# Kernel tuning notes

Hardware: AMD Instinct MI355X
Metric: run time of the kernel (lower is better)

## Reference

```python
import jax, jax.numpy as jnp
import numpy as np

DIM = 1024
HEADS = 16
DIM_HEAD = 64
INNER = HEADS * DIM_HEAD  # 1024
B, N = 4, 1024
SCALE = DIM_HEAD ** -0.5


def _layernorm(t, g, b, eps=1e-5):
    mu = jnp.mean(t, axis=-1, keepdims=True)
    var = jnp.var(t, axis=-1, keepdims=True)
    return (t - mu) * jax.lax.rsqrt(var + eps) * g + b


def setup_inputs() -> dict:
    key = jax.random.key(0)
    ks = jax.random.split(key, 8)
    return {
        "x": jax.random.normal(ks[0], (B, N, DIM), dtype=jnp.float32),
        "y": jax.random.normal(ks[1], (B, N, DIM), dtype=jnp.float32),
        "gx": jnp.ones((DIM,), jnp.float32),
        "bx": jnp.zeros((DIM,), jnp.float32),
        "gy": jnp.ones((DIM,), jnp.float32),
        "by": jnp.zeros((DIM,), jnp.float32),
        "Wqkv_x": jax.random.normal(ks[2], (DIM, 3 * INNER), jnp.float32) * 0.02,
        "Wqkv_y": jax.random.normal(ks[3], (DIM, 3 * INNER), jnp.float32) * 0.02,
        "Wout_x": jax.random.normal(ks[4], (INNER, DIM), jnp.float32) * 0.02,
        "bout_x": jnp.zeros((DIM,), jnp.float32),
        "Wout_y": jax.random.normal(ks[5], (INNER, DIM), jnp.float32) * 0.02,
        "bout_y": jnp.zeros((DIM,), jnp.float32),
    }


def _split_heads(t):
    b, n, _ = t.shape
    return t.reshape(b, n, HEADS, DIM_HEAD).transpose(0, 2, 1, 3)  # b h n d


def reference(x, y, gx, bx, gy, by, Wqkv_x, Wqkv_y, Wout_x, bout_x, Wout_y, bout_y):
    xn = _layernorm(x, gx, bx)
    yn = _layernorm(y, gy, by)
    qx, kx, vx = [_split_heads(t) for t in jnp.split(xn @ Wqkv_x, 3, axis=-1)]
    qy, ky, vy = [_split_heads(t) for t in jnp.split(yn @ Wqkv_y, 3, axis=-1)]
    # concat along HEADS dim -> 2h heads; each stream's heads attend within that stream
    q = jnp.concatenate([qx, qy], axis=1)
    k = jnp.concatenate([kx, ky], axis=1)
    v = jnp.concatenate([vx, vy], axis=1)
    dots = jnp.einsum('bhid,bhjd->bhij', q, k) * SCALE  # [B, 2h, N, N]
    attn = jax.nn.softmax(dots, axis=-1)
    out = jnp.einsum('bhij,bhjd->bhid', attn, v)  # [B, 2h, N, d]
    xo = out[:, :HEADS]  # original code uses the x-chunk for BOTH outputs (faithful)
    xo = xo.transpose(0, 2, 1, 3).reshape(xo.shape[0], xo.shape[2], INNER)  # b n (h d)
    out_x = xo @ Wout_x + bout_x
    out_y = xo @ Wout_y + bout_y
    return (out_x, out_y)
```

## Files before the change

kernel.cpp:

```cpp
#include <hip/hip_runtime.h>

typedef __attribute__((ext_vector_type(8))) short s16x8;
typedef __attribute__((ext_vector_type(4))) float f32x4;
typedef unsigned short u16;

#define DEV __device__ __forceinline__

DEV u16 f2bf(float f) {
    unsigned u = __builtin_bit_cast(unsigned, f);
    unsigned r = u + 0x7fffu + ((u >> 16) & 1u);
    return (u16)(r >> 16);
}

DEV float exp2a(float x) {
    float r;
    asm("v_exp_f32 %0, %1" : "=v"(r) : "v"(x));
    return r;
}

DEV unsigned cvtpk(float lo, float hi) {
    unsigned r;
    asm("v_cvt_pk_bf16_f32 %0, %1, %2" : "=v"(r) : "v"(lo), "v"(hi));
    return r;
}

DEV void gload_lds16(const void* g, void* l) {
    __builtin_amdgcn_global_load_lds(
        (const __attribute__((address_space(1))) unsigned int*)g,
        (__attribute__((address_space(3))) unsigned int*)l, 16, 0, 0);
}

DEV f32x4 mfma16(s16x8 a, s16x8 b, f32x4 c) {
    return __builtin_amdgcn_mfma_f32_16x16x32_bf16(a, b, c, 0, 0, 0);
}

template <int N>
DEV void vmwait() {
    asm volatile("s_waitcnt vmcnt(%0)" ::"n"(N) : "memory");
}

__global__ __launch_bounds__(256) void prep_kernel(
    const float* __restrict__ x, const float* __restrict__ g,
    const float* __restrict__ b, u16* __restrict__ xn,
    const float* __restrict__ Wqkv, const float* __restrict__ Woutx,
    const float* __restrict__ Wouty, u16* __restrict__ wqkv_t,
    u16* __restrict__ wout_t) {
    __shared__ float tile[64][68];
    const int t = threadIdx.x;
    const int bid = blockIdx.x;

    if (bid < 4096) {
        const int row = bid;
        const float4 v = *(const float4*)(x + (size_t)row * 1024 + t * 4);
        float s1 = v.x + v.y + v.z + v.w;
        float s2 = v.x * v.x + v.y * v.y + v.z * v.z + v.w * v.w;
#pragma unroll
        for (int d = 1; d < 64; d <<= 1) {
            s1 += __shfl_xor(s1, d);
            s2 += __shfl_xor(s2, d);
        }
        float* red = &tile[0][0];
        if ((t & 63) == 0) { red[(t >> 6) * 2] = s1; red[(t >> 6) * 2 + 1] = s2; }
        __syncthreads();
        s1 = red[0] + red[2] + red[4] + red[6];
        s2 = red[1] + red[3] + red[5] + red[7];
        const float mu = s1 * (1.0f / 1024.0f);
        const float var = s2 * (1.0f / 1024.0f) - mu * mu;
        const float rs = rsqrtf(var + 1e-5f);
        const float4 gv = *(const float4*)(g + t * 4);
        const float4 bv = *(const float4*)(b + t * 4);
        ushort4 o;
        o.x = f2bf((v.x - mu) * rs * gv.x + bv.x);
        o.y = f2bf((v.y - mu) * rs * gv.y + bv.y);
        o.z = f2bf((v.z - mu) * rs * gv.z + bv.z);
        o.w = f2bf((v.w - mu) * rs * gv.w + bv.w);
        *(ushort4*)(xn + (size_t)row * 1024 + t * 4) = o;
        return;
    }

    const float* src;
    u16* d0;
    int ld, n0, k0;
    if (bid < 4096 + 768) {
        const int idx = bid - 4096;
        src = Wqkv; d0 = wqkv_t; ld = 3072;
        n0 = (idx % 48) * 64; k0 = (idx / 48) * 64;
    } else {
        const int idx = bid - 4096 - 768;
        const int z = idx >> 8, rem = idx & 255;
        src = (z == 0) ? Woutx : Wouty;
        d0 = wout_t + (size_t)z * 1024 * 1024; ld = 1024;
        n0 = (rem & 15) * 64; k0 = (rem >> 4) * 64;
    }
    const int kl = t >> 4, nl = (t & 15) * 4;
#pragma unroll
    for (int p = 0; p < 4; ++p) {
        float4 v = *(const float4*)(src + (size_t)(k0 + kl + p * 16) * ld + n0 + nl);
        tile[kl + p * 16][nl + 0] = v.x;
        tile[kl + p * 16][nl + 1] = v.y;
        tile[kl + p * 16][nl + 2] = v.z;
        tile[kl + p * 16][nl + 3] = v.w;
    }
    __syncthreads();
    const int nl2 = t >> 2, kc = (t & 3) * 16;
    __align__(16) u16 tmp[16];
#pragma unroll
    for (int j = 0; j < 16; ++j) tmp[j] = f2bf(tile[kc + j][nl2]);
    u16* d = d0 + (size_t)(n0 + nl2) * 1024 + k0 + kc;
    ((uint4*)d)[0] = ((const uint4*)tmp)[0];
    ((uint4*)d)[1] = ((const uint4*)tmp)[1];
}

__global__ __launch_bounds__(512, 2) void gemm1k(const u16* __restrict__ A,
                                                 const u16* __restrict__ B,
                                                 u16* __restrict__ Qb, u16* __restrict__ Kb,
                                                 u16* __restrict__ Vt) {
    constexpr int MQ = 2, NQ = 3, HA = 32, HB = 48, TM = 64, TN = 96;
    constexpr int CHA = 1024, CHBF = 1536;
    constexpr int NI = 8;

    __shared__ __align__(16) u16 As[2 * 2 * CHA * 8];
    __shared__ __align__(16) u16 Bs[2 * CHBF * 8];

    const int tid = threadIdx.x, lane = tid & 63;
    const int wave = tid >> 6;
    const int wm = wave >> 1, wn = wave & 1;
    const int lr = lane & 15, cg = lane >> 4;

    const int bid = blockIdx.x;
    const int bid2 = (bid & 7) * 32 + (bid >> 3);
    const int bxi = bid2 & 15, byi = bid2 >> 4;
    const int m0 = byi * 256, n0 = bxi * 192;

    const u16* __restrict__ Ag = A + (size_t)m0 * 1024;
    const u16* __restrict__ Bg = B + (size_t)n0 * 1024;

    f32x4 acc[2 * MQ][2 * NQ] = {};

#define STG_A(b, h, t)                                                              \
    do {                                                                            \
        _Pragma("unroll") for (int u = 0; u < 2; ++u) {                             \
            const int idx = u * 512 + tid;                                          \
            const int loc = idx >> 3, pp = idx & 7;                                 \
            const int row = (loc & 127) | ((h)*128);                                \
            gload_lds16(Ag + (size_t)row * 1024 + (t)*64 + ((pp ^ (row & 7)) << 3), \
                        &As[(((b)*2 + (h)) * CHA + idx) * 8]);                      \
        }                                                                           \
    } while (0)
#define STG_B(b, t)                                                                 \
    do {                                                                            \
        _Pragma("unroll") for (int u = 0; u < 3; ++u) {                             \
            const int idx = u * 512 + tid;                                          \
            const int row = idx >> 3, pp = idx & 7;                                 \
            gload_lds16(Bg + (size_t)row * 1024 + (t)*64 + ((pp ^ (row & 7)) << 3), \
                        &Bs[((b)*CHBF + idx) * 8]);                                 \
        }                                                                           \
    } while (0)

#define LDA(bb, lm, dst)                                                            \
    _Pragma("unroll") for (int mf = 0; mf < MQ; ++mf)                               \
        _Pragma("unroll") for (int ks = 0; ks < 2; ++ks) {                          \
            const int grow = wm * 64 + (lm)*32 + mf * 16 + lr;                      \
            dst[mf][ks] = *(const s16x8*)&As[((((bb)*2 + (grow >> 7)) * CHA) +      \
                                              (grow & 127) * 8 +                    \
                                              ((cg + ks * 4) ^ (lr & 7))) * 8];     \
        }

#define LDB(bb, ln, dst)                                                            \
    _Pragma("unroll") for (int nf = 0; nf < NQ; ++nf)                               \
        _Pragma("unroll") for (int ks = 0; ks < 2; ++ks) {                          \
            const int rr = wn * TN + (ln)*HB + nf * 16 + lr;                        \
            dst[nf][ks] = *(const s16x8*)&Bs[((bb)*CHBF + rr * 8 +                  \
                                              ((cg + ks * 4) ^ (lr & 7))) * 8];     \
        }

#define MM(lm, ln, A_, B_)                                                          \
    __builtin_amdgcn_s_setprio(1);                                                  \
    _Pragma("unroll") for (int mf = 0; mf < MQ; ++mf)                               \
        _Pragma("unroll") for (int nf = 0; nf < NQ; ++nf)                           \
            _Pragma("unroll") for (int ks = 0; ks < 2; ++ks)                        \
                acc[(lm)*MQ + mf][(ln)*NQ + nf] = mfma16(                           \
                    A_[mf][ks], B_[nf][ks], acc[(lm)*MQ + mf][(ln)*NQ + nf]);       \
    __builtin_amdgcn_s_setprio(0);

#define BAR() asm volatile("s_barrier" ::: "memory")

    STG_A(0, 0, 0);
    STG_A(0, 1, 0);
    STG_B(0, 0);
    STG_A(1, 0, 1);
    STG_B(1, 1);
    vmwait<5>();
    BAR();

    s16x8 va[MQ][2];
    s16x8 vb0[NQ][2], vb1[NQ][2];

#pragma unroll 1
    for (int i = 0; i < NI - 1; ++i) {
        const int t1 = 2 * i + 1, t2 = 2 * i + 2, t3 = 2 * i + 3;
        LDA(0, 0, va); LDB(0, 0, vb0); STG_A(1, 1, t1); BAR(); MM(0, 0, va, vb0);
        LDB(0, 1, vb1);                                 BAR(); MM(0, 1, va, vb1);
        LDA(0, 1, va);                 STG_A(0, 0, t2); BAR(); MM(1, 0, va, vb0);
        STG_B(0, t2); vmwait<5>();                      BAR(); MM(1, 1, va, vb1);
        LDA(1, 0, va); LDB(1, 0, vb0); STG_A(0, 1, t2); BAR(); MM(0, 0, va, vb0);
        LDB(1, 1, vb1);                                 BAR(); MM(0, 1, va, vb1);
        LDA(1, 1, va);                 STG_A(1, 0, t3); BAR(); MM(1, 0, va, vb0);
        STG_B(1, t3); vmwait<5>();                      BAR(); MM(1, 1, va, vb1);
    }
    LDA(0, 0, va); LDB(0, 0, vb0); STG_A(1, 1, 15); BAR(); MM(0, 0, va, vb0);
    LDB(0, 1, vb1);                                 BAR(); MM(0, 1, va, vb1);
    LDA(0, 1, va);                                  BAR(); MM(1, 0, va, vb0);
    vmwait<0>();                                    BAR(); MM(1, 1, va, vb1);
    LDA(1, 0, va); LDB(1, 0, vb0); MM(0, 0, va, vb0);
    LDB(1, 1, vb1);                MM(0, 1, va, vb1);
    LDA(1, 1, va);                 MM(1, 0, va, vb0);
    MM(1, 1, va, vb1);

#undef STG_A
#undef STG_B
#undef LDA
#undef LDB
#undef MM
#undef BAR

#pragma unroll
    for (int am = 0; am < 2 * MQ; ++am) {
        const int lm = am / MQ, mf = am % MQ;
        const int rowb = m0 + wm * TM + lm * HA + mf * 16 + cg * 4;
        const int bb2 = rowb >> 10, ii = rowb & 1023;
#pragma unroll
        for (int an = 0; an < 2 * NQ; ++an) {
            const int ln = an / NQ, nf = an % NQ;
            const int col = n0 + wn * TN + ln * HB + nf * 16 + lr;
            const int which = col >> 10, hd = col & 1023;
            const int h = hd >> 6, dd = hd & 63;
            if (which == 2) {
                ushort4 pk;
                pk.x = f2bf(acc[am][an][0]);
                pk.y = f2bf(acc[am][an][1]);
                pk.z = f2bf(acc[am][an][2]);
                pk.w = f2bf(acc[am][an][3]);
                *(ushort4*)(Vt + (size_t)((bb2 << 4) + h) * 65536 + dd * 1024 + ii) = pk;
            } else {
                u16* dst = (which == 0) ? Qb : Kb;
                const float sc = (which == 0) ? 0.18033688011112042f : 1.0f;
#pragma unroll
                for (int r = 0; r < 4; ++r)
                    dst[(size_t)(((bb2 << 4) + h) * 1024 + ii + r) * 64 + dd] =
                        f2bf(acc[am][an][r] * sc);
            }
        }
    }
}

template <int BN, int WM, int EPI>
__global__ __launch_bounds__(512, 2) void gemm8(const u16* __restrict__ A,
                                                const u16* __restrict__ B,
                                                u16* __restrict__ Qb, u16* __restrict__ Kb,
                                                u16* __restrict__ Vb,
                                                const float* __restrict__ bx,
                                                const float* __restrict__ by,
                                                float* __restrict__ out, int NBX) {
    constexpr int BM = 256, WN = 8 / WM;
    constexpr int TM = BM / WM, TN = BN / WN;
    constexpr int MQ = TM / 32, NQ = TN / 32;
    constexpr int HA = TM / 2, HB = TN / 2;
    constexpr int CHA = 1024;
    constexpr int CHB = BN * 4;
    constexpr int GA = 2, GB = CHB / 512;
    constexpr int NI = 8;

    __shared__ __align__(16) u16 As[2 * 2 * CHA * 8];
    __shared__ __align__(16) u16 Bs[2 * 2 * CHB * 8];

    const int tid = threadIdx.x, lane = tid & 63;
    const int wave = tid >> 6;
    const int wm = wave / WN, wn = wave % WN;
    const int lr = lane & 15, cg = lane >> 4;

    const int nwg = NBX * 16;
    const int bid = blockIdx.x;
    const int bid2 = (bid & 7) * (nwg >> 3) + (bid >> 3);
    const int bxi = bid2 % NBX, byi = bid2 / NBX;
    const int m0 = byi * 256, n0 = bxi * BN;

    const u16* __restrict__ Ag = A + (size_t)m0 * 1024;
    const u16* __restrict__ Bg = B + (size_t)n0 * 1024;

    f32x4 acc[2 * MQ][2 * NQ] = {};

#define STG_A(b, h, t)                                                              \
    do {                                                                            \
        _Pragma("unroll") for (int u = 0; u < GA; ++u) {                            \
            const int idx = u * 512 + tid;                                          \
            const int loc = idx >> 3, pp = idx & 7;                                 \
            const int row = (loc & (HA - 1)) | ((h)*HA) | ((loc / HA) * 2 * HA);    \
            gload_lds16(Ag + (size_t)row * 1024 + (t)*64 + ((pp ^ (row & 7)) << 3), \
                        &As[(((b)*2 + (h)) * CHA + idx) * 8]);                      \
        }                                                                           \
    } while (0)
#define STG_B(b, h, t)                                                              \
    do {                                                                            \
        _Pragma("unroll") for (int u = 0; u < GB; ++u) {                            \
            const int idx = u * 512 + tid;                                          \
            const int loc = idx >> 3, pp = idx & 7;                                 \
            const int row = (loc & (HB - 1)) | ((h)*HB) | ((loc / HB) * 2 * HB);    \
            gload_lds16(Bg + (size_t)row * 1024 + (t)*64 + ((pp ^ (row & 7)) << 3), \
                        &Bs[(((b)*2 + (h)) * CHB + idx) * 8]);                      \
        }                                                                           \
    } while (0)

#define LDA(bb, lm, dst)                                                            \
    _Pragma("unroll") for (int mf = 0; mf < MQ; ++mf)                               \
        _Pragma("unroll") for (int ks = 0; ks < 2; ++ks)                            \
            dst[mf][ks] = *(const s16x8*)&As[((((bb)*2 + (lm)) * CHA) +             \
                                              (mf * 16 + lr + wm * HA) * 8 +        \
                                              ((cg + ks * 4) ^ (lr & 7))) * 8];

#define LDB(bb, ln, dst)                                                            \
    _Pragma("unroll") for (int nf = 0; nf < NQ; ++nf)                               \
        _Pragma("unroll") for (int ks = 0; ks < 2; ++ks)                            \
            dst[nf][ks] = *(const s16x8*)&Bs[((((bb)*2 + (ln)) * CHB) +             \
                                              (nf * 16 + lr + wn * HB) * 8 +        \
                                              ((cg + ks * 4) ^ (lr & 7))) * 8];

#define MM(lm, ln, A_, B_)                                                          \
    __builtin_amdgcn_s_setprio(1);                                                  \
    _Pragma("unroll") for (int mf = 0; mf < MQ; ++mf)                               \
        _Pragma("unroll") for (int nf = 0; nf < NQ; ++nf)                           \
            _Pragma("unroll") for (int ks = 0; ks < 2; ++ks)                        \
                acc[(lm)*MQ + mf][(ln)*NQ + nf] = mfma16(                           \
                    A_[mf][ks], B_[nf][ks], acc[(lm)*MQ + mf][(ln)*NQ + nf]);       \
    __builtin_amdgcn_s_setprio(0);

#define BAR() asm volatile("s_barrier" ::: "memory")

    STG_A(0, 0, 0);
    STG_A(0, 1, 0);
    STG_B(0, 0, 0);
    STG_B(0, 1, 0);
    STG_A(1, 0, 1);
    STG_B(1, 0, 1);
    vmwait<GA + GB>();
    BAR();

    s16x8 va[MQ][2];
    s16x8 vb0[NQ][2], vb1[NQ][2];

#pragma unroll 1
    for (int i = 0; i < NI - 1; ++i) {
        const int t1 = 2 * i + 1, t2 = 2 * i + 2, t3 = 2 * i + 3;
        LDA(0, 0, va); LDB(0, 0, vb0); STG_A(1, 1, t1); BAR(); MM(0, 0, va, vb0);
        LDB(0, 1, vb1);                STG_B(1, 1, t1); BAR(); MM(0, 1, va, vb1);
        LDA(0, 1, va);                 STG_A(0, 0, t2); BAR(); MM(1, 0, va, vb0);
        STG_B(0, 0, t2); vmwait<GA + GB>();             BAR(); MM(1, 1, va, vb1);
        LDA(1, 0, va); LDB(1, 0, vb0); STG_A(0, 1, t2); BAR(); MM(0, 0, va, vb0);
        LDB(1, 1, vb1);                STG_B(0, 1, t2); BAR(); MM(0, 1, va, vb1);
        LDA(1, 1, va);                 STG_A(1, 0, t3); BAR(); MM(1, 0, va, vb0);
        STG_B(1, 0, t3); vmwait<GA + GB>();             BAR(); MM(1, 1, va, vb1);
    }
    LDA(0, 0, va); LDB(0, 0, vb0); STG_A(1, 1, 15); BAR(); MM(0, 0, va, vb0);
    LDB(0, 1, vb1);                STG_B(1, 1, 15); BAR(); MM(0, 1, va, vb1);
    LDA(0, 1, va);                                  BAR(); MM(1, 0, va, vb0);
    vmwait<0>();                                    BAR(); MM(1, 1, va, vb1);
    LDA(1, 0, va); LDB(1, 0, vb0); MM(0, 0, va, vb0);
    LDB(1, 1, vb1);                MM(0, 1, va, vb1);
    LDA(1, 1, va);                 MM(1, 0, va, vb0);
    MM(1, 1, va, vb1);

#undef STG_A
#undef STG_B
#undef LDA
#undef LDB
#undef MM
#undef BAR

#pragma unroll
    for (int am = 0; am < 2 * MQ; ++am) {
        const int lm = am / MQ, mf = am % MQ;
        const int rowb = m0 + wm * TM + lm * HA + mf * 16 + cg * 4;
#pragma unroll
        for (int an = 0; an < 2 * NQ; ++an) {
            const int ln = an / NQ, nf = an % NQ;
            const int col = n0 + wn * TN + ln * HB + nf * 16 + lr;
            if (EPI == 0) {
                const int which = col >> 10, hd = col & 1023;
                const int h = hd >> 6, dd = hd & 63;
                u16* dst = (which == 0) ? Qb : (which == 1) ? Kb : Vb;
                const float sc = (which == 0) ? 0.18033688011112042f : 1.0f;
#pragma unroll
                for (int r = 0; r < 4; ++r) {
                    const int tk = rowb + r;
                    const int bb2 = tk >> 10, ii = tk & 1023;
                    dst[(size_t)(((bb2 << 4) + h) * 1024 + ii) * 64 + dd] =
                        f2bf(acc[am][an][r] * sc);
                }
            } else {
                float bias;
                float* ob;
                if (col < 1024) { bias = bx[col]; ob = out + col; }
                else { bias = by[col - 1024]; ob = out + 4194304 + (col - 1024); }
#pragma unroll
                for (int r = 0; r < 4; ++r)
                    ob[(size_t)(rowb + r) * 1024] = acc[am][an][r] + bias;
            }
        }
    }
}

__global__ __launch_bounds__(256) void attn_kernel(const u16* __restrict__ Q,
                                                   const u16* __restrict__ Kg,
                                                   const u16* __restrict__ Vt,
                                                   u16* __restrict__ xo) {
    __shared__ __align__(16) u16 Ks[3][64 * 64];
    __shared__ __align__(16) u16 Vs[3][64 * 64];
    __shared__ __align__(16) u16 Ps[4][32 * 64];
    const int tid = threadIdx.x, lane = tid & 63, w = tid >> 6;
    const int bid = blockIdx.x;
    const int bh = (bid & 7) * 8 + ((bid >> 3) & 7);
    const int qblk = bid >> 6;
    const u16* Qh = Q + (size_t)bh * 65536;
    const u16* Kh = Kg + (size_t)bh * 65536;
    const u16* Vh = Vt + (size_t)bh * 65536;
    const int lr = lane & 15, cg = lane >> 4;
    const int q0 = qblk * 128 + w * 32;
    u16* Pw = &Ps[w][0];

    s16x8 qf[2][2];
#pragma unroll
    for (int qg = 0; qg < 2; ++qg)
#pragma unroll
        for (int ks = 0; ks < 2; ++ks)
            qf[qg][ks] =
                *(const s16x8*)(Qh + (size_t)(q0 + qg * 16 + lr) * 64 + ks * 32 + cg * 8);

    f32x4 o[2][4] = {};
    float l_s[2] = {0.f, 0.f};
    float m_s[2] = {-3e38f, -3e38f};
    int ba[4];
#pragma unroll
    for (int r = 0; r < 4; ++r) ba[r] = (cg * 4 + r) * 4;

#define STAGEKV(bufi, kv0)                                                               \
    do {                                                                                 \
        _Pragma("unroll") for (int i = 0; i < 2; ++i) {                                  \
            int idx = i * 256 + tid;                                                     \
            int row = idx >> 3, p = idx & 7;                                             \
            gload_lds16(Kh + (size_t)((kv0) + row) * 64 + ((p ^ (row & 7)) << 3),        \
                        &Ks[bufi][idx * 8]);                                             \
            gload_lds16(Vh + (size_t)row * 1024 + (kv0) + ((p ^ (row & 7)) << 3),        \
                        &Vs[bufi][idx * 8]);                                             \
        }                                                                                \
    } while (0)

    STAGEKV(0, 0);
    STAGEKV(1, 64);

    int buf = 0, sbuf = 2;
    for (int t = 0; t < 16; ++t) {
        if (t == 15) { vmwait<0>(); } else { vmwait<4>(); }
        asm volatile("s_barrier" ::: "memory");
        if (t < 14) STAGEKV(sbuf, (t + 2) * 64);

        f32x4 s[2][4] = {};
#pragma unroll
        for (int fn = 0; fn < 4; ++fn) {
            const int r = fn * 16 + lr;
#pragma unroll
            for (int ks = 0; ks < 2; ++ks) {
                const int c = cg + ks * 4;
                s16x8 kf = *(const s16x8*)&Ks[buf][r * 64 + ((c ^ (r & 7)) << 3)];
                s[0][fn] = mfma16(kf, qf[0][ks], s[0][fn]);
                s[1][fn] = mfma16(kf, qf[1][ks], s[1][fn]);
            }
        }

#pragma unroll
        for (int qg = 0; qg < 2; ++qg) {
            float tm = -3e38f;
#pragma unroll
            for (int fn = 0; fn < 4; ++fn)
#pragma unroll
                for (int r = 0; r < 4; ++r) tm = fmaxf(tm, s[qg][fn][r]);
            tm = fmaxf(tm, __shfl_xor(tm, 16));
            tm = fmaxf(tm, __shfl_xor(tm, 32));
            if (!__all(tm <= m_s[qg] + 8.0f)) {
                const float mn = fmaxf(m_s[qg], tm);
                const float corr = exp2a(m_s[qg] - mn);
                m_s[qg] = mn;
                l_s[qg] *= corr;
                f32x4 corr_o;
#pragma unroll
                for (int r = 0; r < 4; ++r)
                    corr_o[r] = __builtin_bit_cast(
                        float,
                        __builtin_amdgcn_ds_bpermute(ba[r], __builtin_bit_cast(int, corr)));
#pragma unroll
                for (int fd = 0; fd < 4; ++fd) o[qg][fd] *= corr_o;
            }
            const float mn = m_s[qg];
            float rs = 0.f;
            const int prow = (qg * 16 + lr) * 64;
#pragma unroll
            for (int fn = 0; fn < 4; ++fn) {
                const float p0 = exp2a(s[qg][fn][0] - mn);
                const float p1 = exp2a(s[qg][fn][1] - mn);
                const float p2 = exp2a(s[qg][fn][2] - mn);
                const float p3 = exp2a(s[qg][fn][3] - mn);
                rs += (p0 + p1) + (p2 + p3);
                uint2 dd;
                dd.x = cvtpk(p0, p1);
                dd.y = cvtpk(p2, p3);
                *(uint2*)(Pw + prow + (((2 * fn + (cg >> 1)) ^ (lr & 7)) << 3) +
                          ((cg & 1) << 2)) = dd;
            }
            rs += __shfl_xor(rs, 16);
            rs += __shfl_xor(rs, 32);
            l_s[qg] += rs;
        }

        s16x8 pf[2][2];
#pragma unroll
        for (int qg = 0; qg < 2; ++qg)
#pragma unroll
            for (int ks = 0; ks < 2; ++ks)
                pf[qg][ks] = *(const s16x8*)(Pw + (qg * 16 + lr) * 64 +
                                             (((4 * ks + cg) ^ (lr & 7)) << 3));
#pragma unroll
        for (int fd = 0; fd < 4; ++fd) {
            const int rr = fd * 16 + lr;
#pragma unroll
            for (int ks = 0; ks < 2; ++ks) {
                const int c = cg + ks * 4;
                s16x8 vf = *(const s16x8*)&Vs[buf][rr * 64 + ((c ^ (rr & 7)) << 3)];
                o[0][fd] = mfma16(pf[0][ks], vf, o[0][fd]);
                o[1][fd] = mfma16(pf[1][ks], vf, o[1][fd]);
            }
        }
        buf = (buf == 2) ? 0 : buf + 1;
        sbuf = (sbuf == 2) ? 0 : sbuf + 1;
    }
#undef STAGEKV

    const int b = bh >> 4, h = bh & 15;
#pragma unroll
    for (int qg = 0; qg < 2; ++qg) {
        f32x4 inv;
#pragma unroll
        for (int r = 0; r < 4; ++r) {
            const float lq = __builtin_bit_cast(
                float, __builtin_amdgcn_ds_bpermute(ba[r], __builtin_bit_cast(int, l_s[qg])));
            inv[r] = 1.0f / lq;
        }
#pragma unroll
        for (int r = 0; r < 4; ++r) {
            const int qrow = q0 + qg * 16 + cg * 4 + r;
#pragma unroll
            for (int fd = 0; fd < 4; ++fd)
                xo[(size_t)(b * 1024 + qrow) * 1024 + h * 64 + fd * 16 + lr] =
                    f2bf(o[qg][fd][r] * inv[r]);
        }
    }
}

extern "C" void kernel_launch(void* const* d_in, const int* in_sizes, int n_in,
                              void* d_out, int out_size, void* d_ws, size_t ws_size,
                              hipStream_t stream) {
    const float* x = (const float*)d_in[0];
    const float* gx = (const float*)d_in[2];
    const float* bxv = (const float*)d_in[3];
    const float* Wqkv = (const float*)d_in[6];
    const float* Woutx = (const float*)d_in[8];
    const float* boutx = (const float*)d_in[9];
    const float* Wouty = (const float*)d_in[10];
    const float* bouty = (const float*)d_in[11];
    float* out = (float*)d_out;

    u16* ws = (u16*)d_ws;
    u16* xn = ws;
    u16* wqkv_t = xn + 4096 * 1024;
    u16* wout_t = wqkv_t + 3072 * 1024;
    u16* Qb = wout_t + 2048 * 1024;
    u16* Kb = Qb + 64 * 1024 * 64;
    u16* Vtb = Kb + 64 * 1024 * 64;
    u16* xob = Vtb + 64 * 1024 * 64;

    prep_kernel<<<4096 + 768 + 512, 256, 0, stream>>>(x, gx, bxv, xn, Wqkv, Woutx,
                                                      Wouty, wqkv_t, wout_t);
    gemm1k<<<256, 512, 0, stream>>>(xn, wqkv_t, Qb, Kb, Vtb);
    attn_kernel<<<512, 256, 0, stream>>>(Qb, Kb, Vtb, xob);
    gemm8<128, 4, 1><<<256, 512, 0, stream>>>(xob, wout_t, nullptr, nullptr, nullptr,
                                              boutx, bouty, out, 16);
}
```

Baseline: 99.16 us.

## Software-pipeline QK^T of next KV tile with softmax/PV of current tile

Restructures the attention inner loop into a two-stage software pipeline: the QK^T MFMAs for tile t+1 are issued before the softmax and PV of tile t, using two score register sets that alternate. KV staging moves to a 4-deep LDS ring buffer so prefetch stays three tiles ahead, and the loop is manually unrolled by two with a prologue and epilogue. The aim is to overlap exp/max work with matrix-core work. In exchange it uses more registers and more LDS, which may lower occupancy.

```diff
diff --git a/kernel.cpp b/kernel.cpp
--- a/kernel.cpp
+++ b/kernel.cpp
@@ -413,8 +413,8 @@
                                                    const u16* __restrict__ Kg,
                                                    const u16* __restrict__ Vt,
                                                    u16* __restrict__ xo) {
-    __shared__ __align__(16) u16 Ks[3][64 * 64];
-    __shared__ __align__(16) u16 Vs[3][64 * 64];
+    __shared__ __align__(16) u16 Ks[4][64 * 64];
+    __shared__ __align__(16) u16 Vs[4][64 * 64];
     __shared__ __align__(16) u16 Ps[4][32 * 64];
     const int tid = threadIdx.x, lane = tid & 63, w = tid >> 6;
     const int bid = blockIdx.x;
@@ -454,94 +454,131 @@
         }                                                                                \
     } while (0)
 
+#define BARR() asm volatile("s_barrier" ::: "memory")
+
+#define QK(kb, sX)                                                                       \
+    _Pragma("unroll") for (int fn = 0; fn < 4; ++fn) {                                   \
+        const int r = fn * 16 + lr;                                                      \
+        _Pragma("unroll") for (int ks = 0; ks < 2; ++ks) {                               \
+            const int c = cg + ks * 4;                                                   \
+            s16x8 kf = *(const s16x8*)&Ks[kb][r * 64 + ((c ^ (r & 7)) << 3)];            \
+            sX[0][fn] = mfma16(kf, qf[0][ks], sX[0][fn]);                                \
+            sX[1][fn] = mfma16(kf, qf[1][ks], sX[1][fn]);                                \
+        }                                                                                \
+    }
+
+#define ZERO(sX)                                                                         \
+    _Pragma("unroll") for (int z = 0; z < 4; ++z) {                                      \
+        sX[0][z] = f32x4{0.f, 0.f, 0.f, 0.f};                                            \
+        sX[1][z] = f32x4{0.f, 0.f, 0.f, 0.f};                                            \
+    }
+
+#define SMPV(sX, vb)                                                                     \
+    do {                                                                                 \
+        _Pragma("unroll") for (int qg = 0; qg < 2; ++qg) {                               \
+            float tm = -3e38f;                                                           \
+            _Pragma("unroll") for (int fn = 0; fn < 4; ++fn)                             \
+                _Pragma("unroll") for (int r = 0; r < 4; ++r)                            \
+                    tm = fmaxf(tm, sX[qg][fn][r]);                                       \
+            tm = fmaxf(tm, __shfl_xor(tm, 16));                                          \
+            tm = fmaxf(tm, __shfl_xor(tm, 32));                                          \
+            if (!__all(tm <= m_s[qg] + 8.0f)) {                                          \
+                const float mn = fmaxf(m_s[qg], tm);                                     \
+                const float corr = exp2a(m_s[qg] - mn);                                  \
+                m_s[qg] = mn;                                                            \
+                l_s[qg] *= corr;                                                         \
+                f32x4 corr_o;                                                            \
+                _Pragma("unroll") for (int r = 0; r < 4; ++r)                            \
+                    corr_o[r] = __builtin_bit_cast(                                      \
+                        float, __builtin_amdgcn_ds_bpermute(                             \
+                                   ba[r], __builtin_bit_cast(int, corr)));               \
+                _Pragma("unroll") for (int fd = 0; fd < 4; ++fd) o[qg][fd] *= corr_o;    \
+            }                                                                            \
+            const float mn = m_s[qg];                                                    \
+            float rs = 0.f;                                                              \
+            const int prow = (qg * 16 + lr) * 64;                                       \
+            _Pragma("unroll") for (int fn = 0; fn < 4; ++fn) {                           \
+                const float p0 = exp2a(sX[qg][fn][0] - mn);                              \
+                const float p1 = exp2a(sX[qg][fn][1] - mn);                              \
+                const float p2 = exp2a(sX[qg][fn][2] - mn);                              \
+                const float p3 = exp2a(sX[qg][fn][3] - mn);                              \
+                rs += (p0 + p1) + (p2 + p3);                                             \
+                uint2 dd;                                                                \
+                dd.x = cvtpk(p0, p1);                                                    \
+                dd.y = cvtpk(p2, p3);                                                    \
+                *(uint2*)(Pw + prow + (((2 * fn + (cg >> 1)) ^ (lr & 7)) << 3) +         \
+                          ((cg & 1) << 2)) = dd;                                         \
+            }                                                                            \
+            rs += __shfl_xor(rs, 16);                                                    \
+            rs += __shfl_xor(rs, 32);                                                    \
+            l_s[qg] += rs;                                                               \
+        }                                                                                \
+        s16x8 pf[2][2];                                                                  \
+        _Pragma("unroll") for (int qg = 0; qg < 2; ++qg)                                 \
+            _Pragma("unroll") for (int ks = 0; ks < 2; ++ks)                             \
+                pf[qg][ks] = *(const s16x8*)(Pw + (qg * 16 + lr) * 64 +                  \
+                                             (((4 * ks + cg) ^ (lr & 7)) << 3));         \
+        _Pragma("unroll") for (int fd = 0; fd < 4; ++fd) {                               \
+            const int rr = fd * 16 + lr;                                                 \
+            _Pragma("unroll") for (int ks = 0; ks < 2; ++ks) {                           \
+                const int c = cg + ks * 4;                                               \
+                s16x8 vf = *(const s16x8*)&Vs[vb][rr * 64 + ((c ^ (rr & 7)) << 3)];      \
+                o[0][fd] = mfma16(pf[0][ks], vf, o[0][fd]);                              \
+                o[1][fd] = mfma16(pf[1][ks], vf, o[1][fd]);                              \
+            }                                                                            \
+        }                                                                                \
+    } while (0)
+
+    f32x4 sA[2][4], sB[2][4];
+
     STAGEKV(0, 0);
     STAGEKV(1, 64);
-
-    int buf = 0, sbuf = 2;
-    for (int t = 0; t < 16; ++t) {
-        if (t == 15) { vmwait<0>(); } else { vmwait<4>(); }
-        asm volatile("s_barrier" ::: "memory");
-        if (t < 14) STAGEKV(sbuf, (t + 2) * 64);
-
-        f32x4 s[2][4] = {};
-#pragma unroll
-        for (int fn = 0; fn < 4; ++fn) {
-            const int r = fn * 16 + lr;
-#pragma unroll
-            for (int ks = 0; ks < 2; ++ks) {
-                const int c = cg + ks * 4;
-                s16x8 kf = *(const s16x8*)&Ks[buf][r * 64 + ((c ^ (r & 7)) << 3)];
-                s[0][fn] = mfma16(kf, qf[0][ks], s[0][fn]);
-                s[1][fn] = mfma16(kf, qf[1][ks], s[1][fn]);
-            }
-        }
-
-#pragma unroll
-        for (int qg = 0; qg < 2; ++qg) {
-            float tm = -3e38f;
-#pragma unroll
-            for (int fn = 0; fn < 4; ++fn)
-#pragma unroll
-                for (int r = 0; r < 4; ++r) tm = fmaxf(tm, s[qg][fn][r]);
-            tm = fmaxf(tm, __shfl_xor(tm, 16));
-            tm = fmaxf(tm, __shfl_xor(tm, 32));
-            if (!__all(tm <= m_s[qg] + 8.0f)) {
-                const float mn = fmaxf(m_s[qg], tm);
-                const float corr = exp2a(m_s[qg] - mn);
-                m_s[qg] = mn;
-                l_s[qg] *= corr;
-                f32x4 corr_o;
-#pragma unroll
-                for (int r = 0; r < 4; ++r)
-                    corr_o[r] = __builtin_bit_cast(
-                        float,
-                        __builtin_amdgcn_ds_bpermute(ba[r], __builtin_bit_cast(int, corr)));
-#pragma unroll
-                for (int fd = 0; fd < 4; ++fd) o[qg][fd] *= corr_o;
-            }
-            const float mn = m_s[qg];
-            float rs = 0.f;
-            const int prow = (qg * 16 + lr) * 64;
-#pragma unroll
-            for (int fn = 0; fn < 4; ++fn) {
-                const float p0 = exp2a(s[qg][fn][0] - mn);
-                const float p1 = exp2a(s[qg][fn][1] - mn);
-                const float p2 = exp2a(s[qg][fn][2] - mn);
-                const float p3 = exp2a(s[qg][fn][3] - mn);
-                rs += (p0 + p1) + (p2 + p3);
-                uint2 dd;
-                dd.x = cvtpk(p0, p1);
-                dd.y = cvtpk(p2, p3);
-                *(uint2*)(Pw + prow + (((2 * fn + (cg >> 1)) ^ (lr & 7)) << 3) +
-                          ((cg & 1) << 2)) = dd;
-            }
-            rs += __shfl_xor(rs, 16);
-            rs += __shfl_xor(rs, 32);
-            l_s[qg] += rs;
-        }
-
-        s16x8 pf[2][2];
-#pragma unroll
-        for (int qg = 0; qg < 2; ++qg)
-#pragma unroll
-            for (int ks = 0; ks < 2; ++ks)
-                pf[qg][ks] = *(const s16x8*)(Pw + (qg * 16 + lr) * 64 +
-                                             (((4 * ks + cg) ^ (lr & 7)) << 3));
-#pragma unroll
-        for (int fd = 0; fd < 4; ++fd) {
-            const int rr = fd * 16 + lr;
-#pragma unroll
-            for (int ks = 0; ks < 2; ++ks) {
-                const int c = cg + ks * 4;
-                s16x8 vf = *(const s16x8*)&Vs[buf][rr * 64 + ((c ^ (rr & 7)) << 3)];
-                o[0][fd] = mfma16(pf[0][ks], vf, o[0][fd]);
-                o[1][fd] = mfma16(pf[1][ks], vf, o[1][fd]);
-            }
-        }
-        buf = (buf == 2) ? 0 : buf + 1;
-        sbuf = (sbuf == 2) ? 0 : sbuf + 1;
-    }
+    STAGEKV(2, 128);
+    vmwait<8>();
+    BARR();
+    ZERO(sA);
+    QK(0, sA);
+
+#pragma unroll 1
+    for (int tt = 0; tt < 6; ++tt) {
+        const int t0 = 2 * tt;
+        const int b0 = t0 & 3;
+        vmwait<4>();
+        BARR();
+        STAGEKV((b0 + 3) & 3, (t0 + 3) * 64);
+        ZERO(sB);
+        QK((b0 + 1) & 3, sB);
+        SMPV(sA, b0);
+        vmwait<4>();
+        BARR();
+        STAGEKV(b0, (t0 + 4) * 64);
+        ZERO(sA);
+        QK((b0 + 2) & 3, sA);
+        SMPV(sB, (b0 + 1) & 3);
+    }
+    vmwait<4>();
+    BARR();
+    STAGEKV(3, 15 * 64);
+    ZERO(sB);
+    QK(1, sB);
+    SMPV(sA, 0);
+    vmwait<4>();
+    BARR();
+    ZERO(sA);
+    QK(2, sA);
+    SMPV(sB, 1);
+    vmwait<0>();
+    BARR();
+    ZERO(sB);
+    QK(3, sB);
+    SMPV(sA, 2);
+    SMPV(sB, 3);
+
 #undef STAGEKV
+#undef BARR
+#undef QK
+#undef ZERO
+#undef SMPV
 
     const int b = bh >> 4, h = bh & 15;
 #pragma unroll
```

Result: no change. 100.1 us (+0.9%).
